# Performance work log

Hardware: AMD Instinct MI355X
Metric: run time of the kernel (lower is better)

## Reference

```python
import jax, jax.numpy as jnp
import numpy as np

DIM = 128
GROUPS = [1, 2, 2, 3]


def setup_inputs() -> dict:
    key = jax.random.key(0)
    ks = jax.random.split(key, 8)
    c = DIM
    def p(k, shape, scale=0.02):
        return jax.random.normal(k, shape, dtype=jnp.float32) * scale
    return {
        "x": jax.random.normal(ks[0], (8, c, 128, 128), dtype=jnp.float32),
        "temperature": jnp.ones((4, 1, 1), dtype=jnp.float32),
        "w_qkv": p(ks[1], (3 * c, c)),            # Conv2d(dim, 3*dim, 1), bias=False
        "w_dw": p(ks[2], (3 * c, 1, 3, 3)),        # depthwise 3x3, groups=3*dim
        "w_proj": p(ks[3], (c, c)),                # Conv2d(dim, dim, 1), bias=False
        "w_gate": p(ks[4], (c, c)),                # Intra gatingConv (Conv1d k=1)
        "b_gate": jnp.zeros((c,), jnp.float32),
        "w_down": p(ks[5], (c // 2, c)),           # Intra down
        "b_down": jnp.zeros((c // 2,), jnp.float32),
        "w_up": p(ks[6], (c, c // 2)),             # Intra up
        "b_up": jnp.zeros((c,), jnp.float32),
    }


def _group_sizes(c):
    total = sum(GROUPS)
    sizes = [int(r / total * c) for r in GROUPS]
    sizes[-1] += c - sum(sizes)
    return sizes


def _forward(x, temperature, w_qkv, w_dw, w_proj, w_gate, b_gate,
             w_down, b_down, w_up, b_up):
    b, c, h, w = x.shape
    L = h * w
    # qkv = dwconv3x3(conv1x1(x))
    qkv = jnp.einsum('bchw,oc->bohw', x, w_qkv)
    qkv = jax.lax.conv_general_dilated(
        qkv, w_dw, (1, 1), 'SAME', feature_group_count=3 * c,
        dimension_numbers=('NCHW', 'OIHW', 'NCHW'))
    q, k, v = jnp.split(qkv.reshape(b, 3 * c, L), 3, axis=1)
    # ReGroup: sort channels by mean q activation (descending), split into groups
    channel_mean = q.mean(axis=(0, 2))            # (c,)
    idx = jnp.argsort(-channel_mean)
    q, k, v = q[:, idx], k[:, idx], v[:, idx]
    sizes = _group_sizes(c)
    outs, caches, cache_means = [], [], []
    start = 0
    for i, g in enumerate(sizes):
        qg = q[:, start:start + g]
        kg = k[:, start:start + g]
        vg = v[:, start:start + g]
        start += g
        qn = qg / jnp.maximum(jnp.linalg.norm(qg, axis=-1, keepdims=True), 1e-12)
        kn = kg / jnp.maximum(jnp.linalg.norm(kg, axis=-1, keepdims=True), 1e-12)
        attn = jax.nn.softmax(
            jnp.einsum('bcl,bdl->bcd', qn, kn) * temperature[i, 0, 0], axis=-1)
        outs.append(jnp.einsum('bcd,bdl->bcl', attn, vg))   # (b, g, L)
        tc = jax.lax.stop_gradient(qn + kn)                 # detached cache
        caches.append(tc)
        # per-group mean over L, channel-tiled/padded to c (for cache update)
        gm = tc.mean(axis=-1)                               # (b, g)
        rep = max(1, c // g)
        gm = jnp.tile(gm, (1, rep))
        gm = gm[:, :c] if gm.shape[1] >= c else jnp.pad(gm, ((0, 0), (0, c - gm.shape[1])))
        cache_means.append(gm)
    out_all = jnp.concatenate(outs, axis=1)       # (b, c, L)
    tmp_caches = jnp.concatenate(caches, axis=1)  # (b, c, L)
    # CalculateCurrentLayerCache: bilinear upsample of (1,1) map == broadcast
    s = int(L ** 0.5 + 0.9999)
    acc = sum(cache_means) / float(len(cache_means))        # (b, c)
    qv_cache = jnp.broadcast_to((acc * 0.9)[:, :, None, None], (b, c, s, s))
    # Intra cache modulation: gated = gelu(conv(x1+x2)) * (x1+x2); up(down(gated))
    sxy = out_all + tmp_caches
    gating = jax.nn.gelu(jnp.einsum('bcl,oc->bol', sxy, w_gate) + b_gate[:, None],
                         approximate=False)
    gated = gating * sxy
    mod = jnp.einsum('bcl,oc->bol', gated, w_down) + b_down[:, None]
    mod = jnp.einsum('bcl,oc->bol', mod, w_up) + b_up[:, None]
    out_all = mod + out_all
    out_all = jnp.einsum('bchw,oc->bohw', out_all.reshape(b, c, h, w), w_proj)
    return out_all, qv_cache


def reference(x, temperature, w_qkv, w_dw, w_proj, w_gate, b_gate,
              w_down, b_down, w_up, b_up):
    return _forward(x, temperature, w_qkv, w_dw, w_proj, w_gate, b_gate,
                    w_down, b_down, w_up, b_up)
```

## Files before the change

### kernel.cpp

```cpp
#include <hip/hip_runtime.h>
#include <math.h>

#define B_ 8
#define C_ 128
#define O3_ 384
#define H_ 128
#define W_ 128
#define L_ 16384
#define NS_ 64
#define MAXP_ 2304

template<int KD, int OT, int MODE>
__global__ __launch_bounds__(256) void gemm_k(
    const float* __restrict__ Wt, const float* __restrict__ bias,
    const float* __restrict__ Xa, const float* __restrict__ E0,
    float* __restrict__ Y)
{
    constexpr int RO = OT / 16;
    __shared__ float sW[32][OT + 4];
    __shared__ float sX[32][128];
    const int tid = threadIdx.x;
    const int tx = tid & 15, ty = tid >> 4;
    const int lB = blockIdx.x * 128;
    const int oB = blockIdx.y * OT;
    const int Mtot = gridDim.y * OT;
    const int b = blockIdx.z;
    const size_t xbase = (size_t)b * KD * L_ + lB;

    float acc[RO][8];
#pragma unroll
    for (int i = 0; i < RO; i++)
#pragma unroll
        for (int j = 0; j < 8; j++) acc[i][j] = 0.f;

    for (int kc = 0; kc < KD; kc += 32) {
#pragma unroll
        for (int p = 0; p < 4; p++) {
            int f4 = tid + p * 256;
            int kk = f4 >> 5, c4 = f4 & 31;
            float4 v = *reinterpret_cast<const float4*>(&Xa[xbase + (size_t)(kc + kk) * L_ + c4 * 4]);
            *reinterpret_cast<float4*>(&sX[kk][c4 * 4]) = v;
        }
#pragma unroll
        for (int p = 0; p < OT / 8; p++) {
            int id = tid + p * 256;
            int o = id >> 5, kk = id & 31;
            sW[kk][o] = Wt[(size_t)(oB + o) * KD + kc + kk];
        }
        __syncthreads();
#pragma unroll 8
        for (int kk = 0; kk < 32; kk++) {
            float xv[8], wv[8];
            *reinterpret_cast<float4*>(&xv[0]) = *reinterpret_cast<const float4*>(&sX[kk][tx * 4]);
            *reinterpret_cast<float4*>(&xv[4]) = *reinterpret_cast<const float4*>(&sX[kk][64 + tx * 4]);
            *reinterpret_cast<float4*>(&wv[0]) = *reinterpret_cast<const float4*>(&sW[kk][ty * 4]);
            if constexpr (RO == 8)
                *reinterpret_cast<float4*>(&wv[4]) = *reinterpret_cast<const float4*>(&sW[kk][64 + ty * 4]);
#pragma unroll
            for (int i = 0; i < RO; i++)
#pragma unroll
                for (int j = 0; j < 8; j++)
                    acc[i][j] = fmaf(wv[i], xv[j], acc[i][j]);
        }
        __syncthreads();
    }

#pragma unroll
    for (int i = 0; i < RO; i++) {
        const int oo = (i < 4) ? (ty * 4 + i) : (64 + ty * 4 + (i - 4));
        const int o = oB + oo;
        float bv = 0.f;
        if constexpr (MODE != 0) bv = bias[o];
#pragma unroll
        for (int hl = 0; hl < 2; hl++) {
            const int l = lB + hl * 64 + tx * 4;
            const size_t ybase = ((size_t)b * Mtot + o) * L_ + l;
            const size_t ebase = ((size_t)b * C_ + o) * L_ + l;
            float v[4];
#pragma unroll
            for (int j = 0; j < 4; j++) {
                float a = acc[i][hl * 4 + j] + bv;
                if constexpr (MODE == 1) {
                    float sxy = E0[ebase + j];
                    a = 0.5f * a * (1.0f + erff(a * 0.70710678118654752f)) * sxy;
                }
                if constexpr (MODE == 3) a += E0[ebase + j];
                v[j] = a;
            }
            float4 r = {v[0], v[1], v[2], v[3]};
            *reinterpret_cast<float4*>(&Y[ybase]) = r;
        }
    }
}

__global__ __launch_bounds__(256) void dwconv_k(const float* __restrict__ in,
    const float* __restrict__ wdw, float* __restrict__ outp)
{
    __shared__ float tile[10][130];
    const int ch = blockIdx.y, b = blockIdx.z;
    const int y0 = blockIdx.x * 8;
    const int tid = threadIdx.x;
    const size_t base = ((size_t)b * O3_ + ch) * L_;
    for (int id = tid; id < 1300; id += 256) {
        int r = id / 130, cc = id - r * 130;
        int gy = y0 - 1 + r, gx = cc - 1;
        float v = 0.f;
        if (gy >= 0 && gy < H_ && gx >= 0 && gx < W_) v = in[base + (size_t)gy * W_ + gx];
        tile[r][cc] = v;
    }
    __syncthreads();
    const float* wp = wdw + ch * 9;
    const float w0 = wp[0], w1 = wp[1], w2 = wp[2], w3 = wp[3], w4 = wp[4],
                w5 = wp[5], w6 = wp[6], w7 = wp[7], w8 = wp[8];
    const int tx = tid & 127, ty0 = tid >> 7;
#pragma unroll
    for (int rr = 0; rr < 4; rr++) {
        int r = ty0 + rr * 2;
        float s =
            tile[r + 0][tx + 0] * w0 + tile[r + 0][tx + 1] * w1 + tile[r + 0][tx + 2] * w2 +
            tile[r + 1][tx + 0] * w3 + tile[r + 1][tx + 1] * w4 + tile[r + 1][tx + 2] * w5 +
            tile[r + 2][tx + 0] * w6 + tile[r + 2][tx + 1] * w7 + tile[r + 2][tx + 2] * w8;
        outp[base + (size_t)(y0 + r) * W_ + tx] = s;
    }
}

__global__ __launch_bounds__(256) void sums_k(const float* __restrict__ dw,
    float* __restrict__ sumq, float* __restrict__ sumk,
    float* __restrict__ ssq, float* __restrict__ ssk)
{
    const int c = blockIdx.x, b = blockIdx.y, tid = threadIdx.x;
    const float4* qr = reinterpret_cast<const float4*>(dw + ((size_t)b * O3_ + c) * L_);
    const float4* kr = reinterpret_cast<const float4*>(dw + ((size_t)b * O3_ + 128 + c) * L_);
    float sq = 0.f, s2q = 0.f, sk = 0.f, s2k = 0.f;
    for (int i = tid; i < L_ / 4; i += 256) {
        float4 q4 = qr[i], k4 = kr[i];
        sq += (q4.x + q4.y) + (q4.z + q4.w);
        sk += (k4.x + k4.y) + (k4.z + k4.w);
        s2q += q4.x * q4.x + q4.y * q4.y + q4.z * q4.z + q4.w * q4.w;
        s2k += k4.x * k4.x + k4.y * k4.y + k4.z * k4.z + k4.w * k4.w;
    }
    __shared__ float sm[4][256];
    sm[0][tid] = sq; sm[1][tid] = sk; sm[2][tid] = s2q; sm[3][tid] = s2k;
    __syncthreads();
    for (int st = 128; st > 0; st >>= 1) {
        if (tid < st) {
            sm[0][tid] += sm[0][tid + st]; sm[1][tid] += sm[1][tid + st];
            sm[2][tid] += sm[2][tid + st]; sm[3][tid] += sm[3][tid + st];
        }
        __syncthreads();
    }
    if (tid == 0) {
        sumq[b * 128 + c] = sm[0][0]; sumk[b * 128 + c] = sm[1][0];
        ssq[b * 128 + c]  = sm[2][0]; ssk[b * 128 + c]  = sm[3][0];
    }
}

__global__ void combine_k(const float* __restrict__ sumq, const float* __restrict__ sumk,
    const float* __restrict__ ssq, const float* __restrict__ ssk,
    int* __restrict__ idxp, float* __restrict__ rqc, float* __restrict__ rkc,
    float* __restrict__ gm)
{
    const int t = threadIdx.x;
    __shared__ double cms[128];
    double s = 0.0;
    for (int b = 0; b < B_; b++) s += (double)sumq[b * 128 + t];
    cms[t] = s;
    float rqv[B_], rkv[B_];
    for (int b = 0; b < B_; b++) {
        rqv[b] = 1.f / fmaxf(sqrtf(ssq[b * 128 + t]), 1e-12f);
        rkv[b] = 1.f / fmaxf(sqrtf(ssk[b * 128 + t]), 1e-12f);
        rqc[b * 128 + t] = rqv[b];
        rkc[b * 128 + t] = rkv[b];
    }
    __syncthreads();
    const double mv = cms[t];
    int r = 0;
    for (int j = 0; j < 128; j++) {
        double o = cms[j];
        if (o > mv || (o == mv && j < t)) r++;
    }
    idxp[r] = t;
    for (int b = 0; b < B_; b++)
        gm[b * 128 + r] = (rqv[b] * sumq[b * 128 + t] + rkv[b] * sumk[b * 128 + t]) * (1.0f / L_);
}

template<int G>
__global__ __launch_bounds__(256) void score_k(const float* __restrict__ dw, const int* __restrict__ idxp,
    int start, int gi, float* __restrict__ spart)
{
    constexpr int TS = G / 16;
    const int split = blockIdx.x, b = blockIdx.y;
    const int tid = threadIdx.x, tx = tid & 15, ty = tid >> 4;
    __shared__ float sQ[G][66];
    __shared__ float sK[G][66];
    __shared__ int sc[G];
    if (tid < G) sc[tid] = idxp[start + tid];
    __syncthreads();

    float acc[TS][TS];
#pragma unroll
    for (int i = 0; i < TS; i++)
#pragma unroll
        for (int j = 0; j < TS; j++) acc[i][j] = 0.f;

    const int l0 = split * (L_ / NS_);
    constexpr int LPT = (G * 64) / 256;
    for (int chk = 0; chk < L_ / NS_; chk += 64) {
#pragma unroll
        for (int i = 0; i < LPT; i++) {
            int id = tid + i * 256;
            int row = id >> 6, lc = id & 63;
            size_t base = ((size_t)b * O3_ + sc[row]) * L_ + l0 + chk + lc;
            sQ[row][lc] = dw[base];
            sK[row][lc] = dw[base + (size_t)128 * L_];
        }
        __syncthreads();
#pragma unroll
        for (int kk = 0; kk < 64; kk++) {
            float qv[TS], kv[TS];
#pragma unroll
            for (int j = 0; j < TS; j++) { qv[j] = sQ[ty * TS + j][kk]; kv[j] = sK[tx * TS + j][kk]; }
#pragma unroll
            for (int i = 0; i < TS; i++)
#pragma unroll
                for (int j = 0; j < TS; j++)
                    acc[i][j] = fmaf(qv[i], kv[j], acc[i][j]);
        }
        __syncthreads();
    }
    float* op = spart + (((size_t)(b * 4 + gi)) * NS_ + split) * MAXP_;
#pragma unroll
    for (int i = 0; i < TS; i++)
#pragma unroll
        for (int j = 0; j < TS; j++)
            op[(ty * TS + i) * G + tx * TS + j] = acc[i][j];
}

__global__ __launch_bounds__(256) void softmax_k(const float* __restrict__ spart,
    const float* __restrict__ rqc, const float* __restrict__ rkc, const int* __restrict__ idxp,
    const float* __restrict__ temp, float* __restrict__ attn)
{
    const int gi = blockIdx.x, b = blockIdx.y;
    const int g = (gi == 0) ? 16 : (gi == 3 ? 48 : 32);
    const int start = (gi == 0) ? 0 : (gi == 1 ? 16 : (gi == 2 ? 48 : 80));
    __shared__ float S[MAXP_];
    __shared__ int sidx[48];
    if (threadIdx.x < g) sidx[threadIdx.x] = idxp[start + threadIdx.x];
    __syncthreads();
    const float tv = temp[gi];
    for (int p = threadIdx.x; p < g * g; p += 256) {
        float s = 0.f;
        const float* sp = spart + ((size_t)(b * 4 + gi)) * NS_ * MAXP_ + p;
        for (int k = 0; k < NS_; k++) s += sp[(size_t)k * MAXP_];
        int cc = p / g, dd = p - cc * g;
        S[p] = s * rqc[b * 128 + sidx[cc]] * rkc[b * 128 + sidx[dd]] * tv;
    }
    __syncthreads();
    const int wv = threadIdx.x >> 6, lane = threadIdx.x & 63;
    for (int r = wv; r < g; r += 4) {
        float val = (lane < g) ? S[r * g + lane] : -1e30f;
        float mx = val;
        for (int m = 32; m > 0; m >>= 1) mx = fmaxf(mx, __shfl_xor(mx, m));
        float e = (lane < g) ? expf(val - mx) : 0.f;
        float sum = e;
        for (int m = 32; m > 0; m >>= 1) sum += __shfl_xor(sum, m);
        if (lane < g) attn[((size_t)(b * 4 + gi)) * MAXP_ + r * g + lane] = e / sum;
    }
}

template<int G>
__global__ __launch_bounds__(256) void av_k(const float* __restrict__ dw, const int* __restrict__ idxp,
    const float* __restrict__ rqc, const float* __restrict__ rkc,
    const float* __restrict__ attn, int start, int gi,
    float* __restrict__ outall, float* __restrict__ sxy)
{
    const int b = blockIdx.y;
    const int l = blockIdx.x * 256 + threadIdx.x;
    __shared__ float A[G * G];
    __shared__ int cv[G];
    __shared__ float rqs[G], rks[G];
    if (threadIdx.x < G) {
        int c0 = idxp[start + threadIdx.x];
        cv[threadIdx.x] = c0;
        rqs[threadIdx.x] = rqc[b * 128 + c0];
        rks[threadIdx.x] = rkc[b * 128 + c0];
    }
    for (int p = threadIdx.x; p < G * G; p += 256)
        A[p] = attn[((size_t)(b * 4 + gi)) * MAXP_ + p];
    __syncthreads();
    float acc[G];
#pragma unroll
    for (int c = 0; c < G; c++) acc[c] = 0.f;
    for (int d = 0; d < G; d++) {
        float vd = dw[((size_t)b * O3_ + 256 + cv[d]) * L_ + l];
#pragma unroll
        for (int c = 0; c < G; c++)
            acc[c] = fmaf(A[c * G + d], vd, acc[c]);
    }
    for (int c = 0; c < G; c++) {
        float q = dw[((size_t)b * O3_ + cv[c]) * L_ + l];
        float k = dw[((size_t)b * O3_ + 128 + cv[c]) * L_ + l];
        size_t ob = ((size_t)b * C_ + start + c) * L_ + l;
        outall[ob] = acc[c];
        sxy[ob] = acc[c] + rqs[c] * q + rks[c] * k;
    }
}

__global__ __launch_bounds__(256) void qvc_k(const float* __restrict__ gm, float* __restrict__ outq)
{
    const int cpos = blockIdx.x, b = blockIdx.y;
    const float* g = gm + b * 128;
    float v = g[cpos & 15] + g[16 + (cpos & 31)] + g[48 + (cpos & 31)];
    if (cpos < 96) v += g[80 + (cpos % 48)];
    v *= 0.225f;
    float4 vv = {v, v, v, v};
    float4* op = reinterpret_cast<float4*>(outq + ((size_t)b * C_ + cpos) * L_);
    for (int i = threadIdx.x; i < L_ / 4; i += 256) op[i] = vv;
}

extern "C" void kernel_launch(void* const* d_in, const int* in_sizes, int n_in,
                              void* d_out, int out_size, void* d_ws, size_t ws_size,
                              hipStream_t stream)
{
    const float* x     = (const float*)d_in[0];
    const float* temp  = (const float*)d_in[1];
    const float* wqkv  = (const float*)d_in[2];
    const float* wdw   = (const float*)d_in[3];
    const float* wproj = (const float*)d_in[4];
    const float* wgate = (const float*)d_in[5];
    const float* bgate = (const float*)d_in[6];
    const float* wdown = (const float*)d_in[7];
    const float* bdown = (const float*)d_in[8];
    const float* wup   = (const float*)d_in[9];
    const float* bup   = (const float*)d_in[10];
    float* out = (float*)d_out;
    float* ws  = (float*)d_ws;

    float* qkv = ws;
    float* dw  = ws + 50331648ull;
    float* gated = ws;
    float* mod1  = ws + 16777216ull;
    float* out2  = ws + 25165824ull;
    float* sumq = ws + 44500000ull;
    float* sumk = ws + 44501024ull;
    float* ssq  = ws + 44502048ull;
    float* ssk  = ws + 44503072ull;
    float* rqc  = ws + 44504096ull;
    float* rkc  = ws + 44505120ull;
    float* gm   = ws + 44506144ull;
    double* cmd = (double*)(ws + 44508000ull); (void)cmd;
    int*   idxp = (int*)(ws + 44510000ull);
    float* attn = ws + 45003456ull;
    float* spart= ws + 45077184ull;
    float* outall = out;
    float* sxy    = out + 16777216ull;

    gemm_k<128, 128, 0><<<dim3(128, 3, 8), 256, 0, stream>>>(wqkv, nullptr, x, nullptr, qkv);
    dwconv_k<<<dim3(16, 384, 8), 256, 0, stream>>>(qkv, wdw, dw);
    sums_k<<<dim3(128, 8), 256, 0, stream>>>(dw, sumq, sumk, ssq, ssk);
    combine_k<<<1, 128, 0, stream>>>(sumq, sumk, ssq, ssk, idxp, rqc, rkc, gm);
    score_k<16><<<dim3(NS_, 8), 256, 0, stream>>>(dw, idxp, 0, 0, spart);
    score_k<32><<<dim3(NS_, 8), 256, 0, stream>>>(dw, idxp, 16, 1, spart);
    score_k<32><<<dim3(NS_, 8), 256, 0, stream>>>(dw, idxp, 48, 2, spart);
    score_k<48><<<dim3(NS_, 8), 256, 0, stream>>>(dw, idxp, 80, 3, spart);
    softmax_k<<<dim3(4, 8), 256, 0, stream>>>(spart, rqc, rkc, idxp, temp, attn);
    av_k<16><<<dim3(64, 8), 256, 0, stream>>>(dw, idxp, rqc, rkc, attn, 0, 0, outall, sxy);
    av_k<32><<<dim3(64, 8), 256, 0, stream>>>(dw, idxp, rqc, rkc, attn, 16, 1, outall, sxy);
    av_k<32><<<dim3(64, 8), 256, 0, stream>>>(dw, idxp, rqc, rkc, attn, 48, 2, outall, sxy);
    av_k<48><<<dim3(64, 8), 256, 0, stream>>>(dw, idxp, rqc, rkc, attn, 80, 3, outall, sxy);
    gemm_k<128, 128, 1><<<dim3(128, 1, 8), 256, 0, stream>>>(wgate, bgate, sxy, sxy, gated);
    qvc_k<<<dim3(128, 8), 256, 0, stream>>>(gm, out + 16777216ull);
    gemm_k<128, 64, 2><<<dim3(128, 1, 8), 256, 0, stream>>>(wdown, bdown, gated, nullptr, mod1);
    gemm_k<64, 128, 3><<<dim3(128, 1, 8), 256, 0, stream>>>(wup, bup, mod1, outall, out2);
    gemm_k<128, 128, 0><<<dim3(128, 1, 8), 256, 0, stream>>>(wproj, nullptr, out2, nullptr, out);
}
```

Measured before the change: 852.8 us.

## Use split-bf16 MFMA GEMMs with channel-last intermediates and staged attention-value kernel

Replaces the scalar FP32 1x1-conv GEMMs with MFMA bf16 matrix instructions. Each fp32 operand is split into a high and a low bf16 part and three products are summed, which keeps accuracy close to fp32. The intermediate activations move to a channel-last layout: an explicit transpose of x is added, and the attention-value kernel now stages Q/K/V tiles in shared memory and writes channel-last outputs. Scratch buffers are also relocated into the output buffer. The aim is to remove the FP32 ALU bottleneck of the GEMMs, at the cost of an extra transpose pass, scattered epilogue stores and three MFMAs per product.

```diff
diff --git a/kernel.cpp b/kernel.cpp
--- a/kernel.cpp
+++ b/kernel.cpp
@@ -10,85 +10,145 @@
 #define NS_ 64
 #define MAXP_ 2304
 
+typedef float f32x4 __attribute__((ext_vector_type(4)));
+typedef short bf16x8 __attribute__((ext_vector_type(8)));
+
+static __device__ __forceinline__ ushort f2bf(float f) {
+    uint u = __float_as_uint(f);
+    u += 0x7fffu + ((u >> 16) & 1u);
+    return (ushort)(u >> 16);
+}
+static __device__ __forceinline__ float bf2f(ushort h) {
+    return __uint_as_float(((uint)h) << 16);
+}
+
+__global__ __launch_bounds__(256) void transp_k(const float* __restrict__ x, float* __restrict__ xT)
+{
+    __shared__ float t[32][33];
+    const int b = blockIdx.z;
+    const int c0 = blockIdx.y * 32, l0 = blockIdx.x * 32;
+    const int tx = threadIdx.x & 31, ty = threadIdx.x >> 5;
+#pragma unroll
+    for (int i = 0; i < 4; i++) {
+        int c = ty + i * 8;
+        t[c][tx] = x[((size_t)b * C_ + c0 + c) * L_ + l0 + tx];
+    }
+    __syncthreads();
+#pragma unroll
+    for (int i = 0; i < 4; i++) {
+        int l = ty + i * 8;
+        xT[((size_t)b * L_ + l0 + l) * C_ + c0 + tx] = t[tx][l];
+    }
+}
+
 template<int KD, int OT, int MODE>
-__global__ __launch_bounds__(256) void gemm_k(
+__global__ __launch_bounds__(256) void mgemm_k(
     const float* __restrict__ Wt, const float* __restrict__ bias,
     const float* __restrict__ Xa, const float* __restrict__ E0,
     float* __restrict__ Y)
 {
-    constexpr int RO = OT / 16;
-    __shared__ float sW[32][OT + 4];
-    __shared__ float sX[32][128];
+    constexpr int NR = OT / 32;
+    __shared__ short sAh[128][40];
+    __shared__ short sAl[128][40];
+    __shared__ short sBh[OT][40];
+    __shared__ short sBl[OT][40];
     const int tid = threadIdx.x;
-    const int tx = tid & 15, ty = tid >> 4;
+    const int lane = tid & 63;
+    const int wid = tid >> 6;
+    const int wr = wid >> 1, wc = wid & 1;
     const int lB = blockIdx.x * 128;
     const int oB = blockIdx.y * OT;
-    const int Mtot = gridDim.y * OT;
+    const int ON = gridDim.y * OT;
     const int b = blockIdx.z;
-    const size_t xbase = (size_t)b * KD * L_ + lB;
-
-    float acc[RO][8];
-#pragma unroll
-    for (int i = 0; i < RO; i++)
-#pragma unroll
-        for (int j = 0; j < 8; j++) acc[i][j] = 0.f;
+    const int ln15 = lane & 15, lg = lane >> 4;
+
+    f32x4 acc[4][NR];
+#pragma unroll
+    for (int m = 0; m < 4; m++)
+#pragma unroll
+        for (int n = 0; n < NR; n++)
+#pragma unroll
+            for (int r = 0; r < 4; r++) acc[m][n][r] = 0.f;
 
     for (int kc = 0; kc < KD; kc += 32) {
 #pragma unroll
         for (int p = 0; p < 4; p++) {
             int f4 = tid + p * 256;
-            int kk = f4 >> 5, c4 = f4 & 31;
-            float4 v = *reinterpret_cast<const float4*>(&Xa[xbase + (size_t)(kc + kk) * L_ + c4 * 4]);
-            *reinterpret_cast<float4*>(&sX[kk][c4 * 4]) = v;
-        }
-#pragma unroll
-        for (int p = 0; p < OT / 8; p++) {
-            int id = tid + p * 256;
-            int o = id >> 5, kk = id & 31;
-            sW[kk][o] = Wt[(size_t)(oB + o) * KD + kc + kk];
+            int l = f4 >> 3, c4 = f4 & 7;
+            float4 v = *reinterpret_cast<const float4*>(
+                &Xa[((size_t)b * L_ + lB + l) * KD + kc + c4 * 4]);
+            ushort h0 = f2bf(v.x), h1 = f2bf(v.y), h2 = f2bf(v.z), h3 = f2bf(v.w);
+            ushort g0 = f2bf(v.x - bf2f(h0)), g1 = f2bf(v.y - bf2f(h1));
+            ushort g2 = f2bf(v.z - bf2f(h2)), g3 = f2bf(v.w - bf2f(h3));
+            uint* ah = reinterpret_cast<uint*>(&sAh[l][0]);
+            uint* al = reinterpret_cast<uint*>(&sAl[l][0]);
+            ah[c4 * 2 + 0] = (uint)h0 | ((uint)h1 << 16);
+            ah[c4 * 2 + 1] = (uint)h2 | ((uint)h3 << 16);
+            al[c4 * 2 + 0] = (uint)g0 | ((uint)g1 << 16);
+            al[c4 * 2 + 1] = (uint)g2 | ((uint)g3 << 16);
+        }
+#pragma unroll
+        for (int p = 0; p < OT / 32; p++) {
+            int f4 = tid + p * 256;
+            int o = f4 >> 3, c4 = f4 & 7;
+            float4 v = *reinterpret_cast<const float4*>(
+                &Wt[(size_t)(oB + o) * KD + kc + c4 * 4]);
+            ushort h0 = f2bf(v.x), h1 = f2bf(v.y), h2 = f2bf(v.z), h3 = f2bf(v.w);
+            ushort g0 = f2bf(v.x - bf2f(h0)), g1 = f2bf(v.y - bf2f(h1));
+            ushort g2 = f2bf(v.z - bf2f(h2)), g3 = f2bf(v.w - bf2f(h3));
+            uint* bh = reinterpret_cast<uint*>(&sBh[o][0]);
+            uint* bl = reinterpret_cast<uint*>(&sBl[o][0]);
+            bh[c4 * 2 + 0] = (uint)h0 | ((uint)h1 << 16);
+            bh[c4 * 2 + 1] = (uint)h2 | ((uint)h3 << 16);
+            bl[c4 * 2 + 0] = (uint)g0 | ((uint)g1 << 16);
+            bl[c4 * 2 + 1] = (uint)g2 | ((uint)g3 << 16);
         }
         __syncthreads();
-#pragma unroll 8
-        for (int kk = 0; kk < 32; kk++) {
-            float xv[8], wv[8];
-            *reinterpret_cast<float4*>(&xv[0]) = *reinterpret_cast<const float4*>(&sX[kk][tx * 4]);
-            *reinterpret_cast<float4*>(&xv[4]) = *reinterpret_cast<const float4*>(&sX[kk][64 + tx * 4]);
-            *reinterpret_cast<float4*>(&wv[0]) = *reinterpret_cast<const float4*>(&sW[kk][ty * 4]);
-            if constexpr (RO == 8)
-                *reinterpret_cast<float4*>(&wv[4]) = *reinterpret_cast<const float4*>(&sW[kk][64 + ty * 4]);
-#pragma unroll
-            for (int i = 0; i < RO; i++)
-#pragma unroll
-                for (int j = 0; j < 8; j++)
-                    acc[i][j] = fmaf(wv[i], xv[j], acc[i][j]);
-        }
+        bf16x8 Ah[4], Al[4], Bh[NR], Bl[NR];
+#pragma unroll
+        for (int m = 0; m < 4; m++) {
+            int row = wr * 64 + m * 16 + ln15;
+            Ah[m] = *reinterpret_cast<const bf16x8*>(&sAh[row][lg * 8]);
+            Al[m] = *reinterpret_cast<const bf16x8*>(&sAl[row][lg * 8]);
+        }
+#pragma unroll
+        for (int n = 0; n < NR; n++) {
+            int row = wc * (OT / 2) + n * 16 + ln15;
+            Bh[n] = *reinterpret_cast<const bf16x8*>(&sBh[row][lg * 8]);
+            Bl[n] = *reinterpret_cast<const bf16x8*>(&sBl[row][lg * 8]);
+        }
+#pragma unroll
+        for (int m = 0; m < 4; m++)
+#pragma unroll
+            for (int n = 0; n < NR; n++) {
+                acc[m][n] = __builtin_amdgcn_mfma_f32_16x16x32_bf16(Ah[m], Bh[n], acc[m][n], 0, 0, 0);
+                acc[m][n] = __builtin_amdgcn_mfma_f32_16x16x32_bf16(Ah[m], Bl[n], acc[m][n], 0, 0, 0);
+                acc[m][n] = __builtin_amdgcn_mfma_f32_16x16x32_bf16(Al[m], Bh[n], acc[m][n], 0, 0, 0);
+            }
         __syncthreads();
     }
 
 #pragma unroll
-    for (int i = 0; i < RO; i++) {
-        const int oo = (i < 4) ? (ty * 4 + i) : (64 + ty * 4 + (i - 4));
-        const int o = oB + oo;
-        float bv = 0.f;
-        if constexpr (MODE != 0) bv = bias[o];
-#pragma unroll
-        for (int hl = 0; hl < 2; hl++) {
-            const int l = lB + hl * 64 + tx * 4;
-            const size_t ybase = ((size_t)b * Mtot + o) * L_ + l;
-            const size_t ebase = ((size_t)b * C_ + o) * L_ + l;
-            float v[4];
-#pragma unroll
-            for (int j = 0; j < 4; j++) {
-                float a = acc[i][hl * 4 + j] + bv;
-                if constexpr (MODE == 1) {
-                    float sxy = E0[ebase + j];
-                    a = 0.5f * a * (1.0f + erff(a * 0.70710678118654752f)) * sxy;
+    for (int m = 0; m < 4; m++) {
+        const int lg4 = lB + wr * 64 + m * 16 + lg * 4;
+#pragma unroll
+        for (int n = 0; n < NR; n++) {
+            const int o = oB + wc * (OT / 2) + n * 16 + ln15;
+            if constexpr (MODE == 4) {
+                float4 r4 = {acc[m][n][0], acc[m][n][1], acc[m][n][2], acc[m][n][3]};
+                *reinterpret_cast<float4*>(&Y[((size_t)b * ON + o) * L_ + lg4]) = r4;
+            } else {
+                float bv = (MODE != 0) ? bias[o] : 0.f;
+#pragma unroll
+                for (int r = 0; r < 4; r++) {
+                    size_t yi = ((size_t)b * L_ + lg4 + r) * ON + o;
+                    float a = acc[m][n][r] + bv;
+                    if constexpr (MODE == 1)
+                        a = 0.5f * a * (1.f + erff(a * 0.70710678118654752f)) * E0[yi];
+                    if constexpr (MODE == 3) a += E0[yi];
+                    Y[yi] = a;
                 }
-                if constexpr (MODE == 3) a += E0[ebase + j];
-                v[j] = a;
             }
-            float4 r = {v[0], v[1], v[2], v[3]};
-            *reinterpret_cast<float4*>(&Y[ybase]) = r;
         }
     }
 }
@@ -269,40 +329,62 @@
 }
 
 template<int G>
-__global__ __launch_bounds__(256) void av_k(const float* __restrict__ dw, const int* __restrict__ idxp,
+__global__ __launch_bounds__(256) void av2_k(const float* __restrict__ dw, const int* __restrict__ idxp,
     const float* __restrict__ rqc, const float* __restrict__ rkc,
     const float* __restrict__ attn, int start, int gi,
-    float* __restrict__ outall, float* __restrict__ sxy)
-{
+    float* __restrict__ outallT, float* __restrict__ sxyT)
+{
+    constexpr int C4 = G / 4;
+    constexpr int GP = G + 1;
     const int b = blockIdx.y;
-    const int l = blockIdx.x * 256 + threadIdx.x;
-    __shared__ float A[G * G];
+    const int lB = blockIdx.x * 64;
+    const int tid = threadIdx.x;
+    __shared__ float sA[G * GP];
+    __shared__ float sV[64][GP], sQ[64][GP], sK[64][GP];
     __shared__ int cv[G];
     __shared__ float rqs[G], rks[G];
-    if (threadIdx.x < G) {
-        int c0 = idxp[start + threadIdx.x];
-        cv[threadIdx.x] = c0;
-        rqs[threadIdx.x] = rqc[b * 128 + c0];
-        rks[threadIdx.x] = rkc[b * 128 + c0];
-    }
-    for (int p = threadIdx.x; p < G * G; p += 256)
-        A[p] = attn[((size_t)(b * 4 + gi)) * MAXP_ + p];
-    __syncthreads();
-    float acc[G];
-#pragma unroll
-    for (int c = 0; c < G; c++) acc[c] = 0.f;
+    if (tid < G) {
+        int c0 = idxp[start + tid];
+        cv[tid] = c0;
+        rqs[tid] = rqc[b * 128 + c0];
+        rks[tid] = rkc[b * 128 + c0];
+    }
+    for (int p = tid; p < G * G; p += 256) {
+        int cc = p / G, dd = p - cc * G;
+        sA[cc * GP + dd] = attn[((size_t)(b * 4 + gi)) * MAXP_ + p];
+    }
+    __syncthreads();
+    for (int idx = tid; idx < 64 * G; idx += 256) {
+        int l = idx & 63, d = idx >> 6;
+        size_t base = ((size_t)b * O3_ + cv[d]) * L_ + lB + l;
+        sQ[l][d] = dw[base];
+        sK[l][d] = dw[base + (size_t)128 * L_];
+        sV[l][d] = dw[base + (size_t)256 * L_];
+    }
+    __syncthreads();
+    const int strip = tid & 3, l = tid >> 2;
+    float acc[C4];
+#pragma unroll
+    for (int j = 0; j < C4; j++) acc[j] = 0.f;
     for (int d = 0; d < G; d++) {
-        float vd = dw[((size_t)b * O3_ + 256 + cv[d]) * L_ + l];
-#pragma unroll
-        for (int c = 0; c < G; c++)
-            acc[c] = fmaf(A[c * G + d], vd, acc[c]);
-    }
-    for (int c = 0; c < G; c++) {
-        float q = dw[((size_t)b * O3_ + cv[c]) * L_ + l];
-        float k = dw[((size_t)b * O3_ + 128 + cv[c]) * L_ + l];
-        size_t ob = ((size_t)b * C_ + start + c) * L_ + l;
-        outall[ob] = acc[c];
-        sxy[ob] = acc[c] + rqs[c] * q + rks[c] * k;
+        float vd = sV[l][d];
+#pragma unroll
+        for (int j = 0; j < C4; j++)
+            acc[j] = fmaf(sA[(strip * C4 + j) * GP + d], vd, acc[j]);
+    }
+    const size_t ob = ((size_t)b * L_ + lB + l) * C_ + start + strip * C4;
+    float sv[C4];
+#pragma unroll
+    for (int j = 0; j < C4; j++) {
+        int c = strip * C4 + j;
+        sv[j] = acc[j] + rqs[c] * sQ[l][c] + rks[c] * sK[l][c];
+    }
+#pragma unroll
+    for (int j = 0; j < C4; j += 4) {
+        float4 o4 = {acc[j], acc[j + 1], acc[j + 2], acc[j + 3]};
+        float4 s4 = {sv[j], sv[j + 1], sv[j + 2], sv[j + 3]};
+        *reinterpret_cast<float4*>(&outallT[ob + j]) = o4;
+        *reinterpret_cast<float4*>(&sxyT[ob + j]) = s4;
     }
 }
 
@@ -336,41 +418,43 @@
     float* out = (float*)d_out;
     float* ws  = (float*)d_ws;
 
-    float* qkv = ws;
-    float* dw  = ws + 50331648ull;
-    float* gated = ws;
-    float* mod1  = ws + 16777216ull;
-    float* out2  = ws + 25165824ull;
-    float* sumq = ws + 44500000ull;
-    float* sumk = ws + 44501024ull;
-    float* ssq  = ws + 44502048ull;
-    float* ssk  = ws + 44503072ull;
-    float* rqc  = ws + 44504096ull;
-    float* rkc  = ws + 44505120ull;
-    float* gm   = ws + 44506144ull;
-    double* cmd = (double*)(ws + 44508000ull); (void)cmd;
-    int*   idxp = (int*)(ws + 44510000ull);
-    float* attn = ws + 45003456ull;
-    float* spart= ws + 45077184ull;
-    float* outall = out;
-    float* sxy    = out + 16777216ull;
-
-    gemm_k<128, 128, 0><<<dim3(128, 3, 8), 256, 0, stream>>>(wqkv, nullptr, x, nullptr, qkv);
-    dwconv_k<<<dim3(16, 384, 8), 256, 0, stream>>>(qkv, wdw, dw);
-    sums_k<<<dim3(128, 8), 256, 0, stream>>>(dw, sumq, sumk, ssq, ssk);
+    float* qkvCL  = ws;
+    float* xT     = ws + 50331648ull;
+    float* dwCL   = ws + 50331648ull;
+    float* outallT= ws;
+    float* sxyT   = ws + 16777216ull;
+    float* gatedT = ws + 33554432ull;
+    float* mod1T  = ws + 16777216ull;
+    float* out2T  = ws + 25165824ull;
+
+    float* spart = out;
+    float* attn  = out + 4718592ull;
+    float* sumq  = out + 4800000ull;
+    float* sumk  = out + 4801024ull;
+    float* ssq   = out + 4802048ull;
+    float* ssk   = out + 4803072ull;
+    float* rqc   = out + 4804096ull;
+    float* rkc   = out + 4805120ull;
+    float* gm    = out + 4806144ull;
+    int*   idxp  = (int*)(out + 4807168ull);
+
+    transp_k<<<dim3(512, 4, 8), 256, 0, stream>>>(x, xT);
+    mgemm_k<128, 128, 4><<<dim3(128, 3, 8), 256, 0, stream>>>(wqkv, nullptr, xT, nullptr, qkvCL);
+    dwconv_k<<<dim3(16, 384, 8), 256, 0, stream>>>(qkvCL, wdw, dwCL);
+    sums_k<<<dim3(128, 8), 256, 0, stream>>>(dwCL, sumq, sumk, ssq, ssk);
     combine_k<<<1, 128, 0, stream>>>(sumq, sumk, ssq, ssk, idxp, rqc, rkc, gm);
-    score_k<16><<<dim3(NS_, 8), 256, 0, stream>>>(dw, idxp, 0, 0, spart);
-    score_k<32><<<dim3(NS_, 8), 256, 0, stream>>>(dw, idxp, 16, 1, spart);
-    score_k<32><<<dim3(NS_, 8), 256, 0, stream>>>(dw, idxp, 48, 2, spart);
-    score_k<48><<<dim3(NS_, 8), 256, 0, stream>>>(dw, idxp, 80, 3, spart);
+    score_k<16><<<dim3(NS_, 8), 256, 0, stream>>>(dwCL, idxp, 0, 0, spart);
+    score_k<32><<<dim3(NS_, 8), 256, 0, stream>>>(dwCL, idxp, 16, 1, spart);
+    score_k<32><<<dim3(NS_, 8), 256, 0, stream>>>(dwCL, idxp, 48, 2, spart);
+    score_k<48><<<dim3(NS_, 8), 256, 0, stream>>>(dwCL, idxp, 80, 3, spart);
     softmax_k<<<dim3(4, 8), 256, 0, stream>>>(spart, rqc, rkc, idxp, temp, attn);
-    av_k<16><<<dim3(64, 8), 256, 0, stream>>>(dw, idxp, rqc, rkc, attn, 0, 0, outall, sxy);
-    av_k<32><<<dim3(64, 8), 256, 0, stream>>>(dw, idxp, rqc, rkc, attn, 16, 1, outall, sxy);
-    av_k<32><<<dim3(64, 8), 256, 0, stream>>>(dw, idxp, rqc, rkc, attn, 48, 2, outall, sxy);
-    av_k<48><<<dim3(64, 8), 256, 0, stream>>>(dw, idxp, rqc, rkc, attn, 80, 3, outall, sxy);
-    gemm_k<128, 128, 1><<<dim3(128, 1, 8), 256, 0, stream>>>(wgate, bgate, sxy, sxy, gated);
+    av2_k<16><<<dim3(256, 8), 256, 0, stream>>>(dwCL, idxp, rqc, rkc, attn, 0, 0, outallT, sxyT);
+    av2_k<32><<<dim3(256, 8), 256, 0, stream>>>(dwCL, idxp, rqc, rkc, attn, 16, 1, outallT, sxyT);
+    av2_k<32><<<dim3(256, 8), 256, 0, stream>>>(dwCL, idxp, rqc, rkc, attn, 48, 2, outallT, sxyT);
+    av2_k<48><<<dim3(256, 8), 256, 0, stream>>>(dwCL, idxp, rqc, rkc, attn, 80, 3, outallT, sxyT);
+    mgemm_k<128, 128, 1><<<dim3(128, 1, 8), 256, 0, stream>>>(wgate, bgate, sxyT, sxyT, gatedT);
     qvc_k<<<dim3(128, 8), 256, 0, stream>>>(gm, out + 16777216ull);
-    gemm_k<128, 64, 2><<<dim3(128, 1, 8), 256, 0, stream>>>(wdown, bdown, gated, nullptr, mod1);
-    gemm_k<64, 128, 3><<<dim3(128, 1, 8), 256, 0, stream>>>(wup, bup, mod1, outall, out2);
-    gemm_k<128, 128, 0><<<dim3(128, 1, 8), 256, 0, stream>>>(wproj, nullptr, out2, nullptr, out);
-}
+    mgemm_k<128, 64, 2><<<dim3(128, 1, 8), 256, 0, stream>>>(wdown, bdown, gatedT, nullptr, mod1T);
+    mgemm_k<64, 128, 3><<<dim3(128, 1, 8), 256, 0, stream>>>(wup, bup, mod1T, outallT, out2T);
+    mgemm_k<128, 128, 4><<<dim3(128, 1, 8), 256, 0, stream>>>(wproj, nullptr, out2T, nullptr, out);
+}
```

After: 710.0 us. 1.2x faster.
